# Performance work log

Hardware: AMD Instinct MI355X
Metric: run time of the kernel (lower is better)

The kernel has to match this reference:

```python
import jax, jax.numpy as jnp
import numpy as np

B, L, H = 32, 2048, 1024


def setup_inputs() -> dict:
    key = jax.random.key(0)
    k1, k2, k3, k4, k5 = jax.random.split(key, 5)
    stdv = 1.0 / np.sqrt(H)
    return {
        "hidden": jax.random.normal(k1, (B, H), dtype=jnp.float32),
        "encoder_outputs": jax.random.normal(k2, (L, B, H), dtype=jnp.float32),
        "attn_w": jax.random.normal(k3, (H, 2 * H), dtype=jnp.float32) * stdv,
        "attn_b": jax.random.normal(k4, (H,), dtype=jnp.float32) * stdv,
        "v": jax.random.normal(k5, (H,), dtype=jnp.float32) * stdv,
    }


def reference(hidden, encoder_outputs, attn_w, attn_b, v):
    # encoder_outputs: [L, B, H] -> batch-first [B, L, H]
    enc = jnp.transpose(encoder_outputs, (1, 0, 2))
    # Additive (Bahdanau) energies. Split the concat-linear into two GEMMs to
    # avoid materializing the [B, L, 2H] concat:
    #   attn([H_rep, enc]) = hidden @ W_h^T + enc @ W_e^T + b
    w_h, w_e = attn_w[:, :H], attn_w[:, H:]  # each [H, 2H]->[H, H]
    proj = (jnp.einsum("bh,oh->bo", hidden, w_h)[:, None, :]
            + jnp.einsum("blh,oh->blo", enc, w_e)
            + attn_b)
    energy = jnp.tanh(proj)                   # [B, L, H]
    scores = jnp.einsum("blh,h->bl", energy, v)  # [B, L]
    attn = jax.nn.softmax(scores, axis=-1)       # [B, L]
    context = jnp.einsum("bl,blh->bh", attn, enc)  # [B, H]
    return context[None, :, :]  # [1, B, H] matching context.transpose(0,1)
```

## Files before the change

### kernel.cpp

```cpp
#include <hip/hip_runtime.h>
#include <hip/hip_bf16.h>
#include <math.h>

#define Hdim 1024
#define Bdim 32
#define Ldim 2048
#define Mtot (Bdim*Ldim)

typedef __attribute__((ext_vector_type(8))) short short8v;
typedef __attribute__((ext_vector_type(4))) short short4v;
typedef __attribute__((ext_vector_type(4))) float floatx4;

static __device__ inline short f2bf(float f) {
    union { float f; unsigned u; } x; x.f = f;
    unsigned r = x.u + 0x7FFF + ((x.u >> 16) & 1);
    return (short)(r >> 16);
}
static __device__ inline short f2bf_hw(float f) {
    __hip_bfloat16 h = __float2bfloat16(f);
    return *reinterpret_cast<short*>(&h);
}

static __device__ inline float fast_tanh(float x) {
    float t = 2.0f * x;
    t = fminf(fmaxf(t, -30.0f), 30.0f);
    float e = __expf(t);
    return (e - 1.0f) / (e + 1.0f);
}

typedef __attribute__((address_space(1))) const void GVT;
typedef __attribute__((address_space(3))) void LVT;
static __device__ inline void gload_lds16(const void* g, void* l) {
    __builtin_amdgcn_global_load_lds((GVT*)g, (LVT*)l, 16, 0, 0);
}

__global__ __launch_bounds__(256) void convert_w_kernel(
    const float* __restrict__ attn_w, short* __restrict__ w_bf)
{
    int t = blockIdx.x * 256 + threadIdx.x;
    int o = t >> 7;
    int c = t & 127;
    const float* src = attn_w + (size_t)o * 2 * Hdim + Hdim + c * 8;
    float4 a = *(const float4*)(src);
    float4 b = *(const float4*)(src + 4);
    short8v v;
    v[0]=f2bf(a.x); v[1]=f2bf(a.y); v[2]=f2bf(a.z); v[3]=f2bf(a.w);
    v[4]=f2bf(b.x); v[5]=f2bf(b.y); v[6]=f2bf(b.z); v[7]=f2bf(b.w);
    *(short8v*)(w_bf + (size_t)o * Hdim + c * 8) = v;
}

__global__ __launch_bounds__(256) void qproj_kernel(
    const float* __restrict__ hidden, const float* __restrict__ attn_w,
    const float* __restrict__ attn_b, float* __restrict__ qbuf)
{
    int w = blockIdx.x * 4 + (threadIdx.x >> 6);
    int lane = threadIdx.x & 63;
    int o = w >> 5;
    int b = w & 31;
    const float* hrow = hidden + b * Hdim;
    const float* wrow = attn_w + (size_t)o * 2 * Hdim;
    float s = 0.f;
    #pragma unroll
    for (int i = 0; i < 16; i++) s += hrow[lane + i*64] * wrow[lane + i*64];
    s += __shfl_xor(s, 1);  s += __shfl_xor(s, 2);  s += __shfl_xor(s, 4);
    s += __shfl_xor(s, 8);  s += __shfl_xor(s, 16); s += __shfl_xor(s, 32);
    if (lane == 0) qbuf[b * Hdim + o] = s + attn_b[o];
}

#define BM 128
#define BN 128
#define BK 32
#define NKT 32

__global__ __launch_bounds__(256, 4) void scores_kernel(
    const float* __restrict__ enc,
    const short* __restrict__ w_bf,
    const float* __restrict__ qbuf,
    const float* __restrict__ vvec,
    float* __restrict__ spart)
{
    __shared__ short As[2][BM * BK];
    __shared__ short Bs[2][BN * BK];
    __shared__ float sred[BM][2];

    int hw = blockIdx.x;
    int xcd = hw & 7;
    int i5  = hw >> 3;
    int nblk  = i5 & 7;
    int mtile = xcd * 64 + (i5 >> 3);
    int m0 = mtile * BM;
    int n0 = nblk * BN;

    int tid  = threadIdx.x;
    int w    = tid >> 6;
    int l    = tid & 63;
    int wr = w >> 1, wc = w & 1;
    int r15 = l & 15;
    int kc  = l >> 4;
    int rg  = l >> 4;

    int arow = tid >> 2;
    int acol = tid & 3;
    int asw  = (tid >> 3) & 3;
    const float* agp = enc + (size_t)(m0 + arow) * Hdim + acol * 8;
    const int awoff0 = arow * BK + ((acol ^ asw) * 8);
    const int awoff1 = (arow + 64) * BK + ((acol ^ asw) * 8);

    const short* bgp = w_bf + (size_t)(n0 + w*32 + (l >> 2)) * Hdim
                            + (((l & 3) ^ ((l >> 3) & 3)) * 8);

#define STAGE_B(bb, k0) do { \
    gload_lds16(bgp + (k0),                      &Bs[bb][(w*32)      * BK]); \
    gload_lds16(bgp + (k0) + 16*(size_t)Hdim,    &Bs[bb][(w*32 + 16) * BK]); \
} while (0)

    int q = (r15 >> 1) & 3;
    int rc = (kc ^ q) * 8;
#define LDA(mi) (*(const short8v*)(&As[cur][(wr*64 + (mi)*16 + r15) * BK + rc]))
#define LDB(ni) (*(const short8v*)(&Bs[cur][(wc*64 + (ni)*16 + r15) * BK + rc]))

    floatx4 acc[4][4];
    #pragma unroll
    for (int i = 0; i < 4; i++)
        #pragma unroll
        for (int j = 0; j < 4; j++) acc[i][j] = (floatx4){0.f, 0.f, 0.f, 0.f};

    float4 a00, a01, a10, a11;

#define LOAD_A(k0) do { \
    a00 = *(const float4*)(agp + (k0)); \
    a01 = *(const float4*)(agp + (k0) + 4); \
    a10 = *(const float4*)(agp + (k0) + 64*(size_t)Hdim); \
    a11 = *(const float4*)(agp + (k0) + 64*(size_t)Hdim + 4); \
} while (0)
#define CVT_WRITE_A(bb) do { \
    short8v s0, s1; \
    s0[0]=f2bf_hw(a00.x); s0[1]=f2bf_hw(a00.y); s0[2]=f2bf_hw(a00.z); s0[3]=f2bf_hw(a00.w); \
    s0[4]=f2bf_hw(a01.x); s0[5]=f2bf_hw(a01.y); s0[6]=f2bf_hw(a01.z); s0[7]=f2bf_hw(a01.w); \
    s1[0]=f2bf_hw(a10.x); s1[1]=f2bf_hw(a10.y); s1[2]=f2bf_hw(a10.z); s1[3]=f2bf_hw(a10.w); \
    s1[4]=f2bf_hw(a11.x); s1[5]=f2bf_hw(a11.y); s1[6]=f2bf_hw(a11.z); s1[7]=f2bf_hw(a11.w); \
    *(short8v*)(&As[bb][awoff0]) = s0; \
    *(short8v*)(&As[bb][awoff1]) = s1; \
} while (0)

    LOAD_A(0);
    STAGE_B(0, 0);
    CVT_WRITE_A(0);
    __syncthreads();

    #pragma unroll 2
    for (int kt = 0; kt < NKT; kt++) {
        int cur = kt & 1;
        int nxt = cur ^ 1;
        if (kt < NKT - 1) {
            LOAD_A((kt + 1) * BK);
            STAGE_B(nxt, (kt + 1) * BK);
        }
        short8v af[4], bf[4];
        #pragma unroll
        for (int mi = 0; mi < 4; mi++) af[mi] = LDA(mi);
        #pragma unroll
        for (int ni = 0; ni < 4; ni++) bf[ni] = LDB(ni);
        #pragma unroll
        for (int mi = 0; mi < 4; mi++)
            #pragma unroll
            for (int ni = 0; ni < 4; ni++)
                acc[mi][ni] = __builtin_amdgcn_mfma_f32_16x16x32_bf16(af[mi], bf[ni], acc[mi][ni], 0, 0, 0);
        if (kt < NKT - 1) CVT_WRITE_A(nxt);
        __syncthreads();
    }

    #pragma unroll
    for (int mi = 0; mi < 4; mi++) {
        float rs[4] = {0.f, 0.f, 0.f, 0.f};
        #pragma unroll
        for (int ni = 0; ni < 4; ni++) {
            int o = n0 + wc*64 + ni*16 + r15;
            float vo = vvec[o];
            #pragma unroll
            for (int reg = 0; reg < 4; reg++) {
                int trow = wr*64 + mi*16 + rg*4 + reg;
                int b = trow & 31;
                float p = acc[mi][ni][reg] + qbuf[b * Hdim + o];
                rs[reg] += fast_tanh(p) * vo;
            }
        }
        #pragma unroll
        for (int reg = 0; reg < 4; reg++) {
            float s = rs[reg];
            s += __shfl_xor(s, 1); s += __shfl_xor(s, 2);
            s += __shfl_xor(s, 4); s += __shfl_xor(s, 8);
            if (r15 == 0) {
                int trow = wr*64 + mi*16 + rg*4 + reg;
                sred[trow][wc] = s;
            }
        }
    }
    __syncthreads();
    if (tid < BM)
        spart[(size_t)nblk * Mtot + m0 + tid] = sred[tid][0] + sred[tid][1];
#undef STAGE_B
#undef LDA
#undef LDB
#undef LOAD_A
#undef CVT_WRITE_A
}

__global__ __launch_bounds__(256) void softmax_kernel(
    const float* __restrict__ spart,
    float* __restrict__ attn)
{
    int b = blockIdx.x;
    int t = threadIdx.x;
    __shared__ float rmax[4], rsum[4];
    float sv[8];
    float mx = -1e30f;
    #pragma unroll
    for (int i = 0; i < 8; i++) {
        int l = t + i * 256;
        int m = l * Bdim + b;
        float s = 0.f;
        #pragma unroll
        for (int p = 0; p < 8; p++) s += spart[(size_t)p * Mtot + m];
        sv[i] = s;
        mx = fmaxf(mx, s);
    }
    #pragma unroll
    for (int off = 1; off < 64; off <<= 1) mx = fmaxf(mx, __shfl_xor(mx, off));
    if ((t & 63) == 0) rmax[t >> 6] = mx;
    __syncthreads();
    mx = fmaxf(fmaxf(rmax[0], rmax[1]), fmaxf(rmax[2], rmax[3]));
    float sum = 0.f;
    #pragma unroll
    for (int i = 0; i < 8; i++) { sv[i] = __expf(sv[i] - mx); sum += sv[i]; }
    #pragma unroll
    for (int off = 1; off < 64; off <<= 1) sum += __shfl_xor(sum, off);
    if ((t & 63) == 0) rsum[t >> 6] = sum;
    __syncthreads();
    sum = rsum[0] + rsum[1] + rsum[2] + rsum[3];
    float inv = 1.f / sum;
    #pragma unroll
    for (int i = 0; i < 8; i++)
        attn[(size_t)b * Ldim + t + i * 256] = sv[i] * inv;
}

__global__ __launch_bounds__(256) void context_part_kernel(
    const float* __restrict__ enc,
    const float* __restrict__ attn,
    float* __restrict__ cpart)
{
    int b = blockIdx.x & 31;
    int c = blockIdx.x >> 5;
    int t = threadIdx.x;
    float4 acc = {0.f, 0.f, 0.f, 0.f};
    int l0 = c * 32;
    for (int i = 0; i < 32; i++) {
        int l = l0 + i;
        float a = attn[(size_t)b * Ldim + l];
        float4 e = *(const float4*)(enc + (size_t)(l * Bdim + b) * Hdim + t * 4);
        acc.x += a * e.x; acc.y += a * e.y; acc.z += a * e.z; acc.w += a * e.w;
    }
    *(float4*)(cpart + ((size_t)c * Bdim + b) * Hdim + t * 4) = acc;
}

__global__ __launch_bounds__(256) void context_reduce_kernel(
    const float* __restrict__ cpart, float* __restrict__ out)
{
    int idx = blockIdx.x * 256 + threadIdx.x;
    float s = 0.f;
    for (int c = 0; c < 64; c++) s += cpart[(size_t)c * (Bdim * Hdim) + idx];
    out[idx] = s;
}

extern "C" void kernel_launch(void* const* d_in, const int* in_sizes, int n_in,
                              void* d_out, int out_size, void* d_ws, size_t ws_size,
                              hipStream_t stream)
{
    const float* hidden = (const float*)d_in[0];
    const float* enc    = (const float*)d_in[1];
    const float* attn_w = (const float*)d_in[2];
    const float* attn_b = (const float*)d_in[3];
    const float* vvec   = (const float*)d_in[4];
    float* out = (float*)d_out;

    char* ws = (char*)d_ws;
    size_t off = 0;
    short* w_bf   = (short*)(ws + off); off += (size_t)Hdim * Hdim * 2;
    float* qbuf   = (float*)(ws + off); off += (size_t)Bdim * Hdim * 4;
    float* spart  = (float*)(ws + off); off += (size_t)8 * Mtot * 4;
    float* attnp  = (float*)(ws + off); off += (size_t)Mtot * 4;
    float* cpart  = (float*)(ws + off);

    convert_w_kernel<<<512, 256, 0, stream>>>(attn_w, w_bf);
    qproj_kernel<<<8192, 256, 0, stream>>>(hidden, attn_w, attn_b, qbuf);
    scores_kernel<<<4096, 256, 0, stream>>>(enc, w_bf, qbuf, vvec, spart);
    softmax_kernel<<<Bdim, 256, 0, stream>>>(spart, attnp);
    context_part_kernel<<<2048, 256, 0, stream>>>(enc, attnp, cpart);
    context_reduce_kernel<<<128, 256, 0, stream>>>(cpart, out);
}
```

Baseline: 293.2 us.

## Prefetch fp32 A tiles two iterations ahead with explicit vmcnt waits

Moves the fp32 encoder-tile global loads two K-steps ahead, alternating between two register sets, so load latency overlaps with more MFMA work. The full __syncthreads is replaced by explicit s_waitcnt vmcnt/lgkmcnt plus a raw s_barrier. The vmcnt count of 4 lets the newest A prefetch stay in flight while the B LDS loads complete. This costs extra VGPRs and relies on the hand-counted vmcnt values matching the compiler's instruction order. The final iteration skips the barrier entirely.

Result: slower. 337.8 us (+15.2%).

```diff
diff --git a/kernel.cpp b/kernel.cpp
--- a/kernel.cpp
+++ b/kernel.cpp
@@ -108,7 +108,6 @@
 
     const short* bgp = w_bf + (size_t)(n0 + w*32 + (l >> 2)) * Hdim
                             + (((l & 3) ^ ((l >> 3) & 3)) * 8);
-
 #define STAGE_B(bb, k0) do { \
     gload_lds16(bgp + (k0),                      &Bs[bb][(w*32)      * BK]); \
     gload_lds16(bgp + (k0) + 16*(size_t)Hdim,    &Bs[bb][(w*32 + 16) * BK]); \
@@ -125,37 +124,46 @@
         #pragma unroll
         for (int j = 0; j < 4; j++) acc[i][j] = (floatx4){0.f, 0.f, 0.f, 0.f};
 
-    float4 a00, a01, a10, a11;
-
-#define LOAD_A(k0) do { \
-    a00 = *(const float4*)(agp + (k0)); \
-    a01 = *(const float4*)(agp + (k0) + 4); \
-    a10 = *(const float4*)(agp + (k0) + 64*(size_t)Hdim); \
-    a11 = *(const float4*)(agp + (k0) + 64*(size_t)Hdim + 4); \
+    float4 A0_[4], A1_[4];
+
+#define LOAD_SET0(k0) do { \
+    A0_[0] = *(const float4*)(agp + (k0)); \
+    A0_[1] = *(const float4*)(agp + (k0) + 4); \
+    A0_[2] = *(const float4*)(agp + (k0) + 64*(size_t)Hdim); \
+    A0_[3] = *(const float4*)(agp + (k0) + 64*(size_t)Hdim + 4); \
 } while (0)
-#define CVT_WRITE_A(bb) do { \
+#define LOAD_SET1(k0) do { \
+    A1_[0] = *(const float4*)(agp + (k0)); \
+    A1_[1] = *(const float4*)(agp + (k0) + 4); \
+    A1_[2] = *(const float4*)(agp + (k0) + 64*(size_t)Hdim); \
+    A1_[3] = *(const float4*)(agp + (k0) + 64*(size_t)Hdim + 4); \
+} while (0)
+#define CVT_WRITE(SET, bb) do { \
     short8v s0, s1; \
-    s0[0]=f2bf_hw(a00.x); s0[1]=f2bf_hw(a00.y); s0[2]=f2bf_hw(a00.z); s0[3]=f2bf_hw(a00.w); \
-    s0[4]=f2bf_hw(a01.x); s0[5]=f2bf_hw(a01.y); s0[6]=f2bf_hw(a01.z); s0[7]=f2bf_hw(a01.w); \
-    s1[0]=f2bf_hw(a10.x); s1[1]=f2bf_hw(a10.y); s1[2]=f2bf_hw(a10.z); s1[3]=f2bf_hw(a10.w); \
-    s1[4]=f2bf_hw(a11.x); s1[5]=f2bf_hw(a11.y); s1[6]=f2bf_hw(a11.z); s1[7]=f2bf_hw(a11.w); \
+    s0[0]=f2bf_hw(SET[0].x); s0[1]=f2bf_hw(SET[0].y); s0[2]=f2bf_hw(SET[0].z); s0[3]=f2bf_hw(SET[0].w); \
+    s0[4]=f2bf_hw(SET[1].x); s0[5]=f2bf_hw(SET[1].y); s0[6]=f2bf_hw(SET[1].z); s0[7]=f2bf_hw(SET[1].w); \
+    s1[0]=f2bf_hw(SET[2].x); s1[1]=f2bf_hw(SET[2].y); s1[2]=f2bf_hw(SET[2].z); s1[3]=f2bf_hw(SET[2].w); \
+    s1[4]=f2bf_hw(SET[3].x); s1[5]=f2bf_hw(SET[3].y); s1[6]=f2bf_hw(SET[3].z); s1[7]=f2bf_hw(SET[3].w); \
     *(short8v*)(&As[bb][awoff0]) = s0; \
     *(short8v*)(&As[bb][awoff1]) = s1; \
 } while (0)
 
-    LOAD_A(0);
     STAGE_B(0, 0);
-    CVT_WRITE_A(0);
+    LOAD_SET0(0);
+    LOAD_SET1(BK);
+    CVT_WRITE(A0_, 0);
     __syncthreads();
 
     #pragma unroll 2
     for (int kt = 0; kt < NKT; kt++) {
         int cur = kt & 1;
         int nxt = cur ^ 1;
-        if (kt < NKT - 1) {
-            LOAD_A((kt + 1) * BK);
-            STAGE_B(nxt, (kt + 1) * BK);
-        }
+        bool haveB = (kt + 1 < NKT);
+        bool haveA = (kt + 2 < NKT);
+
+        if (haveB) STAGE_B(nxt, (kt + 1) * BK);
+        if (haveA) { if (kt & 1) LOAD_SET1((kt + 2) * BK); else LOAD_SET0((kt + 2) * BK); }
+
         short8v af[4], bf[4];
         #pragma unroll
         for (int mi = 0; mi < 4; mi++) af[mi] = LDA(mi);
@@ -166,8 +174,15 @@
             #pragma unroll
             for (int ni = 0; ni < 4; ni++)
                 acc[mi][ni] = __builtin_amdgcn_mfma_f32_16x16x32_bf16(af[mi], bf[ni], acc[mi][ni], 0, 0, 0);
-        if (kt < NKT - 1) CVT_WRITE_A(nxt);
-        __syncthreads();
+
+        if (haveB) { if ((kt + 1) & 1) CVT_WRITE(A1_, nxt); else CVT_WRITE(A0_, nxt); }
+
+        if (haveB) {
+            if (haveA) asm volatile("s_waitcnt vmcnt(4)" ::: "memory");
+            else       asm volatile("s_waitcnt vmcnt(0)" ::: "memory");
+            asm volatile("s_waitcnt lgkmcnt(0)" ::: "memory");
+            __builtin_amdgcn_s_barrier();
+        }
     }
 
     #pragma unroll
@@ -202,8 +217,9 @@
 #undef STAGE_B
 #undef LDA
 #undef LDB
-#undef LOAD_A
-#undef CVT_WRITE_A
+#undef LOAD_SET0
+#undef LOAD_SET1
+#undef CVT_WRITE
 }
 
 __global__ __launch_bounds__(256) void softmax_kernel(
```

## Stage fp32 encoder tiles directly into LDS and convert to bf16 at fragment load

Applied to the files above, without the earlier changes.

The A operand (encoder outputs) is now copied from global memory into LDS as fp32 with direct global-to-LDS loads, using an XOR swizzle. It is converted to bf16 when each wave reads its MFMA fragments, replacing the old path of loading into registers, converting, then writing to LDS. This frees VGPRs and removes the register round trip, so the A loads can overlap compute the same way the B loads already do. The cost is a doubled LDS footprint for A and repeated conversion work, since each A element is converted by both column waves. Occupancy hint drops from 4 to 3 blocks per CU to fit the larger LDS.

New measurement: 330.7 us. 1.13x slower.

```diff
diff --git a/kernel.cpp b/kernel.cpp
--- a/kernel.cpp
+++ b/kernel.cpp
@@ -72,14 +72,14 @@
 #define BK 32
 #define NKT 32
 
-__global__ __launch_bounds__(256, 4) void scores_kernel(
+__global__ __launch_bounds__(256, 3) void scores_kernel(
     const float* __restrict__ enc,
     const short* __restrict__ w_bf,
     const float* __restrict__ qbuf,
     const float* __restrict__ vvec,
     float* __restrict__ spart)
 {
-    __shared__ short As[2][BM * BK];
+    __shared__ float As[2][BM * BK];
     __shared__ short Bs[2][BN * BK];
     __shared__ float sred[BM][2];
 
@@ -99,24 +99,33 @@
     int kc  = l >> 4;
     int rg  = l >> 4;
 
-    int arow = tid >> 2;
-    int acol = tid & 3;
-    int asw  = (tid >> 3) & 3;
-    const float* agp = enc + (size_t)(m0 + arow) * Hdim + acol * 8;
-    const int awoff0 = arow * BK + ((acol ^ asw) * 8);
-    const int awoff1 = (arow + 64) * BK + ((acol ^ asw) * 8);
+    const float* agp = enc + (size_t)(m0 + w*32 + (l >> 3)) * Hdim
+                           + (((l & 7) ^ ((l >> 3) & 7)) * 4);
+#define STAGE_A(bb, k0) do { \
+    gload_lds16(agp + (k0),                      &As[bb][(w*32)      * BK]); \
+    gload_lds16(agp + (k0) +  8*(size_t)Hdim,    &As[bb][(w*32 +  8) * BK]); \
+    gload_lds16(agp + (k0) + 16*(size_t)Hdim,    &As[bb][(w*32 + 16) * BK]); \
+    gload_lds16(agp + (k0) + 24*(size_t)Hdim,    &As[bb][(w*32 + 24) * BK]); \
+} while (0)
 
     const short* bgp = w_bf + (size_t)(n0 + w*32 + (l >> 2)) * Hdim
                             + (((l & 3) ^ ((l >> 3) & 3)) * 8);
-
 #define STAGE_B(bb, k0) do { \
     gload_lds16(bgp + (k0),                      &Bs[bb][(w*32)      * BK]); \
     gload_lds16(bgp + (k0) + 16*(size_t)Hdim,    &Bs[bb][(w*32 + 16) * BK]); \
 } while (0)
 
-    int q = (r15 >> 1) & 3;
-    int rc = (kc ^ q) * 8;
-#define LDA(mi) (*(const short8v*)(&As[cur][(wr*64 + (mi)*16 + r15) * BK + rc]))
+    int asw = r15 & 7;
+    int ac0 = ((kc * 2)     ^ asw) * 4;
+    int ac1 = ((kc * 2 + 1) ^ asw) * 4;
+#define LDA(mi, dst) do { \
+    int R = (wr*64 + (mi)*16 + r15) * BK; \
+    float4 lo = *(const float4*)(&As[cur][R + ac0]); \
+    float4 hi = *(const float4*)(&As[cur][R + ac1]); \
+    dst[0]=f2bf_hw(lo.x); dst[1]=f2bf_hw(lo.y); dst[2]=f2bf_hw(lo.z); dst[3]=f2bf_hw(lo.w); \
+    dst[4]=f2bf_hw(hi.x); dst[5]=f2bf_hw(hi.y); dst[6]=f2bf_hw(hi.z); dst[7]=f2bf_hw(hi.w); \
+} while (0)
+    int rc = (kc ^ ((r15 >> 1) & 3)) * 8;
 #define LDB(ni) (*(const short8v*)(&Bs[cur][(wc*64 + (ni)*16 + r15) * BK + rc]))
 
     floatx4 acc[4][4];
@@ -125,27 +134,8 @@
         #pragma unroll
         for (int j = 0; j < 4; j++) acc[i][j] = (floatx4){0.f, 0.f, 0.f, 0.f};
 
-    float4 a00, a01, a10, a11;
-
-#define LOAD_A(k0) do { \
-    a00 = *(const float4*)(agp + (k0)); \
-    a01 = *(const float4*)(agp + (k0) + 4); \
-    a10 = *(const float4*)(agp + (k0) + 64*(size_t)Hdim); \
-    a11 = *(const float4*)(agp + (k0) + 64*(size_t)Hdim + 4); \
-} while (0)
-#define CVT_WRITE_A(bb) do { \
-    short8v s0, s1; \
-    s0[0]=f2bf_hw(a00.x); s0[1]=f2bf_hw(a00.y); s0[2]=f2bf_hw(a00.z); s0[3]=f2bf_hw(a00.w); \
-    s0[4]=f2bf_hw(a01.x); s0[5]=f2bf_hw(a01.y); s0[6]=f2bf_hw(a01.z); s0[7]=f2bf_hw(a01.w); \
-    s1[0]=f2bf_hw(a10.x); s1[1]=f2bf_hw(a10.y); s1[2]=f2bf_hw(a10.z); s1[3]=f2bf_hw(a10.w); \
-    s1[4]=f2bf_hw(a11.x); s1[5]=f2bf_hw(a11.y); s1[6]=f2bf_hw(a11.z); s1[7]=f2bf_hw(a11.w); \
-    *(short8v*)(&As[bb][awoff0]) = s0; \
-    *(short8v*)(&As[bb][awoff1]) = s1; \
-} while (0)
-
-    LOAD_A(0);
+    STAGE_A(0, 0);
     STAGE_B(0, 0);
-    CVT_WRITE_A(0);
     __syncthreads();
 
     #pragma unroll 2
@@ -153,12 +143,12 @@
         int cur = kt & 1;
         int nxt = cur ^ 1;
         if (kt < NKT - 1) {
-            LOAD_A((kt + 1) * BK);
+            STAGE_A(nxt, (kt + 1) * BK);
             STAGE_B(nxt, (kt + 1) * BK);
         }
         short8v af[4], bf[4];
         #pragma unroll
-        for (int mi = 0; mi < 4; mi++) af[mi] = LDA(mi);
+        for (int mi = 0; mi < 4; mi++) LDA(mi, af[mi]);
         #pragma unroll
         for (int ni = 0; ni < 4; ni++) bf[ni] = LDB(ni);
         #pragma unroll
@@ -166,7 +156,6 @@
             #pragma unroll
             for (int ni = 0; ni < 4; ni++)
                 acc[mi][ni] = __builtin_amdgcn_mfma_f32_16x16x32_bf16(af[mi], bf[ni], acc[mi][ni], 0, 0, 0);
-        if (kt < NKT - 1) CVT_WRITE_A(nxt);
         __syncthreads();
     }
 
@@ -199,11 +188,10 @@
     __syncthreads();
     if (tid < BM)
         spart[(size_t)nblk * Mtot + m0 + tid] = sred[tid][0] + sred[tid][1];
+#undef STAGE_A
 #undef STAGE_B
 #undef LDA
 #undef LDB
-#undef LOAD_A
-#undef CVT_WRITE_A
 }
 
 __global__ __launch_bounds__(256) void softmax_kernel(
```
